# Optimization experiments

Hardware: AMD Instinct MI355X
Metric: run time of the kernel (lower is better)

## Reference

```python
import jax, jax.numpy as jnp
import numpy as np
import math

B, T, D = 2, 1024, 128
H, DH = 64, 2
SCALE = math.sqrt(DH)
TEMPERATURE = 0.8

def setup_inputs() -> dict:
    key = jax.random.key(0)
    ks = jax.random.split(key, 5)
    inv = 1.0 / math.sqrt(D)
    return {
        "x": jax.random.normal(ks[0], (B, T, D), dtype=jnp.float32),
        "Wq": jax.random.normal(ks[1], (D, D), dtype=jnp.float32) * inv,
        "Wk": jax.random.normal(ks[2], (D, D), dtype=jnp.float32) * inv,
        "Wv": jax.random.normal(ks[3], (D, D), dtype=jnp.float32) * inv,
        "Wo": jax.random.normal(ks[4], (D, D), dtype=jnp.float32) * inv,
    }

def reference(x, Wq, Wk, Wv, Wo):
    b, t, d = x.shape
    # torch nn.Linear(bias=False): y = x @ W.T
    Q = (x @ Wq.T).reshape(b, t, H, DH).transpose(0, 2, 1, 3)  # (B,H,T,dh)
    K = (x @ Wk.T).reshape(b, t, H, DH).transpose(0, 2, 1, 3)
    V = (x @ Wv.T).reshape(b, t, H, DH).transpose(0, 2, 1, 3)
    # scores / sqrt(d_head) / temperature, causal mask (strict upper -> -inf)
    scores = jnp.einsum("bhqd,bhkd->bhqk", Q, K) / (SCALE * TEMPERATURE)
    causal = jnp.triu(jnp.ones((t, t), dtype=bool), k=1)  # True above diagonal
    scores = jnp.where(causal, -jnp.inf, scores)
    attn = jax.nn.softmax(scores, axis=-1)  # dropout is identity in eval mode
    out = jnp.einsum("bhqk,bhkd->bhqd", attn, V)
    out = out.transpose(0, 2, 1, 3).reshape(b, t, d)
    return out @ Wo.T
```

## Files before the change

### kernel.cpp

```cpp
#include <hip/hip_runtime.h>
#include <math.h>

#define Tdim 1024
#define Hh   64

#if __has_builtin(__builtin_amdgcn_exp2f)
#define EXP2(x) __builtin_amdgcn_exp2f(x)
#else
#define EXP2(x) exp2f(x)
#endif

__device__ __constant__ float kQScale = 0.8838834764831844f * 1.4426950408889634f;

__global__ __launch_bounds__(256) void qkv_proj(
    const float* __restrict__ x, const float* __restrict__ Wq,
    const float* __restrict__ Wk, const float* __restrict__ Wv,
    float* __restrict__ Q, float* __restrict__ KV)
{
    __shared__ float xs[16][128];
    __shared__ float Wch[128][36];

    const int tid  = threadIdx.x;
    const int row0 = blockIdx.x * 16;
    const int w    = blockIdx.y;

    {
        const float4* xg = reinterpret_cast<const float4*>(x + (size_t)row0 * 128);
        reinterpret_cast<float4*>(&xs[0][0])[tid]       = xg[tid];
        reinterpret_cast<float4*>(&xs[0][0])[tid + 256] = xg[tid + 256];
    }

    const float* W = (w == 0) ? Wq : (w == 1) ? Wk : Wv;

    const int j0 = tid & 31;
    const int r0 = (tid >> 5) << 1;

    float acc[2][4];
#pragma unroll
    for (int r = 0; r < 2; ++r)
#pragma unroll
        for (int c = 0; c < 4; ++c) acc[r][c] = 0.f;

    for (int ch = 0; ch < 4; ++ch) {
        __syncthreads();
#pragma unroll
        for (int s = 0; s < 4; ++s) {
            const int idx  = tid + s * 256;
            const int rowW = idx >> 3;
            const int c4   = idx & 7;
            *reinterpret_cast<float4*>(&Wch[rowW][c4 * 4]) =
                reinterpret_cast<const float4*>(W + (size_t)rowW * 128 + ch * 32)[c4];
        }
        __syncthreads();

#pragma unroll
        for (int c = 0; c < 8; ++c) {
            const float4 w0 = *reinterpret_cast<const float4*>(&Wch[j0      ][c * 4]);
            const float4 w1 = *reinterpret_cast<const float4*>(&Wch[j0 + 32 ][c * 4]);
            const float4 w2 = *reinterpret_cast<const float4*>(&Wch[j0 + 64 ][c * 4]);
            const float4 w3 = *reinterpret_cast<const float4*>(&Wch[j0 + 96 ][c * 4]);
#pragma unroll
            for (int r = 0; r < 2; ++r) {
                const float4 xv = *reinterpret_cast<const float4*>(&xs[r0 + r][ch * 32 + c * 4]);
                acc[r][0] = fmaf(xv.x, w0.x, fmaf(xv.y, w0.y, fmaf(xv.z, w0.z, fmaf(xv.w, w0.w, acc[r][0]))));
                acc[r][1] = fmaf(xv.x, w1.x, fmaf(xv.y, w1.y, fmaf(xv.z, w1.z, fmaf(xv.w, w1.w, acc[r][1]))));
                acc[r][2] = fmaf(xv.x, w2.x, fmaf(xv.y, w2.y, fmaf(xv.z, w2.z, fmaf(xv.w, w2.w, acc[r][2]))));
                acc[r][3] = fmaf(xv.x, w3.x, fmaf(xv.y, w3.y, fmaf(xv.z, w3.z, fmaf(xv.w, w3.w, acc[r][3]))));
            }
        }
    }

#pragma unroll
    for (int r = 0; r < 2; ++r) {
        const int row = row0 + r0 + r;
        const int bb  = row >> 10;
        const int t   = row & 1023;
#pragma unroll
        for (int jj = 0; jj < 4; ++jj) {
            const int j = j0 + jj * 32;
            const float v = acc[r][jj];
            if (w == 0) {
                Q[(size_t)row * 128 + j] = v * kQScale;
            } else {
                const int h  = j >> 1, dh = j & 1;
                const int bh = bb * Hh + h;
                KV[((size_t)bh * Tdim + t) * 4 + ((w == 1) ? dh : 2 + dh)] = v;
            }
        }
    }
}

__global__ __launch_bounds__(256) void attn(
    const float* __restrict__ Q, const float4* __restrict__ KV,
    float* __restrict__ O)
{
    __shared__ float4 KVs[Tdim];
    const int tid   = threadIdx.x;
    const int c     = blockIdx.x;
    const int bh    = blockIdx.y;
    const int lowb  = c * 64;
    const int highb = (15 - c) * 64;
    const int nk    = highb + 64;

    const float4* KVg = KV + (size_t)bh * Tdim;
    for (int i = tid; i < nk; i += 256) KVs[i] = KVg[i];
    __syncthreads();

    const int sub = tid & 7;
    const int g   = tid >> 3;
    const int lq  = lowb + g * 2;
    const int hq  = highb + g * 2;
    const int b   = bh >> 6, h = bh & 63;

    const float* Qb = Q + (size_t)b * (Tdim * 128) + h * 2;
    float2 q[4];
    q[0] = *reinterpret_cast<const float2*>(Qb + (size_t)(lq    ) * 128);
    q[1] = *reinterpret_cast<const float2*>(Qb + (size_t)(lq + 1) * 128);
    q[2] = *reinterpret_cast<const float2*>(Qb + (size_t)(hq    ) * 128);
    q[3] = *reinterpret_cast<const float2*>(Qb + (size_t)(hq + 1) * 128);

    float l[4]  = {0.f, 0.f, 0.f, 0.f};
    float a0[4] = {0.f, 0.f, 0.f, 0.f};
    float a1[4] = {0.f, 0.f, 0.f, 0.f};

    auto upd = [&](int i, const float4 kv) {
        const float p = EXP2(fmaf(q[i].x, kv.x, q[i].y * kv.y));
        l[i] += p;
        a0[i] = fmaf(p, kv.z, a0[i]);
        a1[i] = fmaf(p, kv.w, a1[i]);
    };

#pragma unroll 2
    for (int k = sub; k < lq; k += 8) {
        const float4 kv = KVs[k];
        upd(0, kv); upd(1, kv); upd(2, kv); upd(3, kv);
    }
    if (sub <= 1) {
        const float4 kv = KVs[lq + sub];
        if (sub == 0) upd(0, kv);
        upd(1, kv);
    }
    int k2 = (lq & ~7) + sub; if (k2 < lq) k2 += 8;
#pragma unroll 4
    for (int k = k2; k < hq; k += 8) {
        const float4 kv = KVs[k];
        upd(2, kv); upd(3, kv);
    }
    if (sub <= 1) {
        const float4 kv = KVs[hq + sub];
        if (sub == 0) upd(2, kv);
        upd(3, kv);
    }

#pragma unroll
    for (int i = 0; i < 4; ++i) {
        l[i]  += __shfl_xor(l[i], 1);  l[i]  += __shfl_xor(l[i], 2);  l[i]  += __shfl_xor(l[i], 4);
        a0[i] += __shfl_xor(a0[i], 1); a0[i] += __shfl_xor(a0[i], 2); a0[i] += __shfl_xor(a0[i], 4);
        a1[i] += __shfl_xor(a1[i], 1); a1[i] += __shfl_xor(a1[i], 2); a1[i] += __shfl_xor(a1[i], 4);
    }

    if (sub == 0) {
        float* Ob = O + (size_t)b * (Tdim * 128) + h * 2;
#pragma unroll
        for (int i = 0; i < 4; ++i) {
            const int row = (i < 2) ? (lq + i) : (hq + i - 2);
            const float rl = 1.0f / l[i];
            *reinterpret_cast<float2*>(Ob + (size_t)row * 128) =
                make_float2(a0[i] * rl, a1[i] * rl);
        }
    }
}

__global__ __launch_bounds__(256) void out_proj(
    const float* __restrict__ Oin, const float* __restrict__ Wo,
    float* __restrict__ out)
{
    __shared__ float xs[16][128];
    __shared__ float Wch[128][36];

    const int tid  = threadIdx.x;
    const int row0 = blockIdx.x * 16;

    {
        const float4* xg = reinterpret_cast<const float4*>(Oin + (size_t)row0 * 128);
        reinterpret_cast<float4*>(&xs[0][0])[tid]       = xg[tid];
        reinterpret_cast<float4*>(&xs[0][0])[tid + 256] = xg[tid + 256];
    }

    const int j0 = tid & 31;
    const int r0 = (tid >> 5) << 1;

    float acc[2][4];
#pragma unroll
    for (int r = 0; r < 2; ++r)
#pragma unroll
        for (int c = 0; c < 4; ++c) acc[r][c] = 0.f;

    for (int ch = 0; ch < 4; ++ch) {
        __syncthreads();
#pragma unroll
        for (int s = 0; s < 4; ++s) {
            const int idx  = tid + s * 256;
            const int rowW = idx >> 3;
            const int c4   = idx & 7;
            *reinterpret_cast<float4*>(&Wch[rowW][c4 * 4]) =
                reinterpret_cast<const float4*>(Wo + (size_t)rowW * 128 + ch * 32)[c4];
        }
        __syncthreads();

#pragma unroll
        for (int c = 0; c < 8; ++c) {
            const float4 w0 = *reinterpret_cast<const float4*>(&Wch[j0      ][c * 4]);
            const float4 w1 = *reinterpret_cast<const float4*>(&Wch[j0 + 32 ][c * 4]);
            const float4 w2 = *reinterpret_cast<const float4*>(&Wch[j0 + 64 ][c * 4]);
            const float4 w3 = *reinterpret_cast<const float4*>(&Wch[j0 + 96 ][c * 4]);
#pragma unroll
            for (int r = 0; r < 2; ++r) {
                const float4 xv = *reinterpret_cast<const float4*>(&xs[r0 + r][ch * 32 + c * 4]);
                acc[r][0] = fmaf(xv.x, w0.x, fmaf(xv.y, w0.y, fmaf(xv.z, w0.z, fmaf(xv.w, w0.w, acc[r][0]))));
                acc[r][1] = fmaf(xv.x, w1.x, fmaf(xv.y, w1.y, fmaf(xv.z, w1.z, fmaf(xv.w, w1.w, acc[r][1]))));
                acc[r][2] = fmaf(xv.x, w2.x, fmaf(xv.y, w2.y, fmaf(xv.z, w2.z, fmaf(xv.w, w2.w, acc[r][2]))));
                acc[r][3] = fmaf(xv.x, w3.x, fmaf(xv.y, w3.y, fmaf(xv.z, w3.z, fmaf(xv.w, w3.w, acc[r][3]))));
            }
        }
    }

#pragma unroll
    for (int r = 0; r < 2; ++r) {
        const int row = row0 + r0 + r;
#pragma unroll
        for (int jj = 0; jj < 4; ++jj) {
            const int j = j0 + jj * 32;
            out[(size_t)row * 128 + j] = acc[r][jj];
        }
    }
}

extern "C" void kernel_launch(void* const* d_in, const int* in_sizes, int n_in,
                              void* d_out, int out_size, void* d_ws, size_t ws_size,
                              hipStream_t stream) {
    const float* x  = (const float*)d_in[0];
    const float* Wq = (const float*)d_in[1];
    const float* Wk = (const float*)d_in[2];
    const float* Wv = (const float*)d_in[3];
    const float* Wo = (const float*)d_in[4];
    float* out = (float*)d_out;

    float* ws = (float*)d_ws;
    float* Q  = ws;
    float* KV = ws + 262144;
    float* O  = ws + 786432;

    qkv_proj<<<dim3(128, 3), 256, 0, stream>>>(x, Wq, Wk, Wv, Q, KV);
    attn<<<dim3(8, 128), 256, 0, stream>>>(Q, (const float4*)KV, O);
    out_proj<<<128, 256, 0, stream>>>(O, Wo, out);
}
```

Measured before the change: 95.34 us.

## Rewrite projection GEMMs as row-per-thread register kernels with column-split grids

Result: slower. 102.8 us (+7.8%).

```diff
diff --git a/kernel.cpp b/kernel.cpp
--- a/kernel.cpp
+++ b/kernel.cpp
@@ -12,80 +12,57 @@
 
 __device__ __constant__ float kQScale = 0.8838834764831844f * 1.4426950408889634f;
 
-__global__ __launch_bounds__(256) void qkv_proj(
+__global__ __launch_bounds__(256, 2) void qkv_proj(
     const float* __restrict__ x, const float* __restrict__ Wq,
     const float* __restrict__ Wk, const float* __restrict__ Wv,
     float* __restrict__ Q, float* __restrict__ KV)
 {
-    __shared__ float xs[16][128];
-    __shared__ float Wch[128][36];
-
-    const int tid  = threadIdx.x;
-    const int row0 = blockIdx.x * 16;
-    const int w    = blockIdx.y;
-
+    const int tid = threadIdx.x;
+    const int row = blockIdx.x * 256 + tid;
+    const int jb  = blockIdx.y * 8;
+    const int mat = blockIdx.z;
+    const float* __restrict__ W = (mat == 0) ? Wq : (mat == 1) ? Wk : Wv;
+
+    float4 xr[32];
     {
-        const float4* xg = reinterpret_cast<const float4*>(x + (size_t)row0 * 128);
-        reinterpret_cast<float4*>(&xs[0][0])[tid]       = xg[tid];
-        reinterpret_cast<float4*>(&xs[0][0])[tid + 256] = xg[tid + 256];
-    }
-
-    const float* W = (w == 0) ? Wq : (w == 1) ? Wk : Wv;
-
-    const int j0 = tid & 31;
-    const int r0 = (tid >> 5) << 1;
-
-    float acc[2][4];
-#pragma unroll
-    for (int r = 0; r < 2; ++r)
-#pragma unroll
-        for (int c = 0; c < 4; ++c) acc[r][c] = 0.f;
-
-    for (int ch = 0; ch < 4; ++ch) {
-        __syncthreads();
-#pragma unroll
-        for (int s = 0; s < 4; ++s) {
-            const int idx  = tid + s * 256;
-            const int rowW = idx >> 3;
-            const int c4   = idx & 7;
-            *reinterpret_cast<float4*>(&Wch[rowW][c4 * 4]) =
-                reinterpret_cast<const float4*>(W + (size_t)rowW * 128 + ch * 32)[c4];
-        }
-        __syncthreads();
-
-#pragma unroll
-        for (int c = 0; c < 8; ++c) {
-            const float4 w0 = *reinterpret_cast<const float4*>(&Wch[j0      ][c * 4]);
-            const float4 w1 = *reinterpret_cast<const float4*>(&Wch[j0 + 32 ][c * 4]);
-            const float4 w2 = *reinterpret_cast<const float4*>(&Wch[j0 + 64 ][c * 4]);
-            const float4 w3 = *reinterpret_cast<const float4*>(&Wch[j0 + 96 ][c * 4]);
-#pragma unroll
-            for (int r = 0; r < 2; ++r) {
-                const float4 xv = *reinterpret_cast<const float4*>(&xs[r0 + r][ch * 32 + c * 4]);
-                acc[r][0] = fmaf(xv.x, w0.x, fmaf(xv.y, w0.y, fmaf(xv.z, w0.z, fmaf(xv.w, w0.w, acc[r][0]))));
-                acc[r][1] = fmaf(xv.x, w1.x, fmaf(xv.y, w1.y, fmaf(xv.z, w1.z, fmaf(xv.w, w1.w, acc[r][1]))));
-                acc[r][2] = fmaf(xv.x, w2.x, fmaf(xv.y, w2.y, fmaf(xv.z, w2.z, fmaf(xv.w, w2.w, acc[r][2]))));
-                acc[r][3] = fmaf(xv.x, w3.x, fmaf(xv.y, w3.y, fmaf(xv.z, w3.z, fmaf(xv.w, w3.w, acc[r][3]))));
-            }
-        }
-    }
-
-#pragma unroll
-    for (int r = 0; r < 2; ++r) {
-        const int row = row0 + r0 + r;
-        const int bb  = row >> 10;
-        const int t   = row & 1023;
-#pragma unroll
-        for (int jj = 0; jj < 4; ++jj) {
-            const int j = j0 + jj * 32;
-            const float v = acc[r][jj];
-            if (w == 0) {
-                Q[(size_t)row * 128 + j] = v * kQScale;
-            } else {
-                const int h  = j >> 1, dh = j & 1;
-                const int bh = bb * Hh + h;
-                KV[((size_t)bh * Tdim + t) * 4 + ((w == 1) ? dh : 2 + dh)] = v;
-            }
+        const float4* xrow = reinterpret_cast<const float4*>(x + (size_t)row * 128);
+#pragma unroll
+        for (int k = 0; k < 32; ++k) xr[k] = xrow[k];
+    }
+
+    float acc[8];
+#pragma unroll
+    for (int c = 0; c < 8; ++c) acc[c] = 0.f;
+
+#pragma unroll
+    for (int c = 0; c < 8; ++c) {
+        const float4* wp = reinterpret_cast<const float4*>(W + (size_t)(jb + c) * 128);
+        float a = 0.f;
+#pragma unroll
+        for (int k = 0; k < 32; ++k) {
+            const float4 wv = wp[k];
+            const float4 xv = xr[k];
+            a = fmaf(xv.x, wv.x, fmaf(xv.y, wv.y, fmaf(xv.z, wv.z, fmaf(xv.w, wv.w, a))));
+        }
+        acc[c] = a;
+    }
+
+    const int b = row >> 10, t = row & 1023;
+    if (mat == 0) {
+        float4 o0 = make_float4(acc[0] * kQScale, acc[1] * kQScale,
+                                acc[2] * kQScale, acc[3] * kQScale);
+        float4 o1 = make_float4(acc[4] * kQScale, acc[5] * kQScale,
+                                acc[6] * kQScale, acc[7] * kQScale);
+        *reinterpret_cast<float4*>(Q + (size_t)row * 128 + jb)     = o0;
+        *reinterpret_cast<float4*>(Q + (size_t)row * 128 + jb + 4) = o1;
+    } else {
+        const int off = (mat == 1) ? 0 : 2;
+#pragma unroll
+        for (int cc = 0; cc < 4; ++cc) {
+            const int h = (jb >> 1) + cc;
+            *reinterpret_cast<float2*>(
+                KV + (((size_t)(b * Hh + h) * Tdim + t) * 4 + off)) =
+                make_float2(acc[2 * cc], acc[2 * cc + 1]);
         }
     }
 }
@@ -171,69 +148,40 @@
     }
 }
 
-__global__ __launch_bounds__(256) void out_proj(
+__global__ __launch_bounds__(256, 2) void out_proj(
     const float* __restrict__ Oin, const float* __restrict__ Wo,
     float* __restrict__ out)
 {
-    __shared__ float xs[16][128];
-    __shared__ float Wch[128][36];
-
-    const int tid  = threadIdx.x;
-    const int row0 = blockIdx.x * 16;
-
+    const int tid = threadIdx.x;
+    const int row = blockIdx.x * 256 + tid;
+    const int jb  = blockIdx.y * 4;
+
+    float4 xr[32];
     {
-        const float4* xg = reinterpret_cast<const float4*>(Oin + (size_t)row0 * 128);
-        reinterpret_cast<float4*>(&xs[0][0])[tid]       = xg[tid];
-        reinterpret_cast<float4*>(&xs[0][0])[tid + 256] = xg[tid + 256];
-    }
-
-    const int j0 = tid & 31;
-    const int r0 = (tid >> 5) << 1;
-
-    float acc[2][4];
-#pragma unroll
-    for (int r = 0; r < 2; ++r)
-#pragma unroll
-        for (int c = 0; c < 4; ++c) acc[r][c] = 0.f;
-
-    for (int ch = 0; ch < 4; ++ch) {
-        __syncthreads();
-#pragma unroll
-        for (int s = 0; s < 4; ++s) {
-            const int idx  = tid + s * 256;
-            const int rowW = idx >> 3;
-            const int c4   = idx & 7;
-            *reinterpret_cast<float4*>(&Wch[rowW][c4 * 4]) =
-                reinterpret_cast<const float4*>(Wo + (size_t)rowW * 128 + ch * 32)[c4];
-        }
-        __syncthreads();
-
-#pragma unroll
-        for (int c = 0; c < 8; ++c) {
-            const float4 w0 = *reinterpret_cast<const float4*>(&Wch[j0      ][c * 4]);
-            const float4 w1 = *reinterpret_cast<const float4*>(&Wch[j0 + 32 ][c * 4]);
-            const float4 w2 = *reinterpret_cast<const float4*>(&Wch[j0 + 64 ][c * 4]);
-            const float4 w3 = *reinterpret_cast<const float4*>(&Wch[j0 + 96 ][c * 4]);
-#pragma unroll
-            for (int r = 0; r < 2; ++r) {
-                const float4 xv = *reinterpret_cast<const float4*>(&xs[r0 + r][ch * 32 + c * 4]);
-                acc[r][0] = fmaf(xv.x, w0.x, fmaf(xv.y, w0.y, fmaf(xv.z, w0.z, fmaf(xv.w, w0.w, acc[r][0]))));
-                acc[r][1] = fmaf(xv.x, w1.x, fmaf(xv.y, w1.y, fmaf(xv.z, w1.z, fmaf(xv.w, w1.w, acc[r][1]))));
-                acc[r][2] = fmaf(xv.x, w2.x, fmaf(xv.y, w2.y, fmaf(xv.z, w2.z, fmaf(xv.w, w2.w, acc[r][2]))));
-                acc[r][3] = fmaf(xv.x, w3.x, fmaf(xv.y, w3.y, fmaf(xv.z, w3.z, fmaf(xv.w, w3.w, acc[r][3]))));
-            }
-        }
-    }
-
-#pragma unroll
-    for (int r = 0; r < 2; ++r) {
-        const int row = row0 + r0 + r;
-#pragma unroll
-        for (int jj = 0; jj < 4; ++jj) {
-            const int j = j0 + jj * 32;
-            out[(size_t)row * 128 + j] = acc[r][jj];
-        }
-    }
+        const float4* xrow = reinterpret_cast<const float4*>(Oin + (size_t)row * 128);
+#pragma unroll
+        for (int k = 0; k < 32; ++k) xr[k] = xrow[k];
+    }
+
+    float acc[4];
+#pragma unroll
+    for (int c = 0; c < 4; ++c) acc[c] = 0.f;
+
+#pragma unroll
+    for (int c = 0; c < 4; ++c) {
+        const float4* wp = reinterpret_cast<const float4*>(Wo + (size_t)(jb + c) * 128);
+        float a = 0.f;
+#pragma unroll
+        for (int k = 0; k < 32; ++k) {
+            const float4 wv = wp[k];
+            const float4 xv = xr[k];
+            a = fmaf(xv.x, wv.x, fmaf(xv.y, wv.y, fmaf(xv.z, wv.z, fmaf(xv.w, wv.w, a))));
+        }
+        acc[c] = a;
+    }
+
+    *reinterpret_cast<float4*>(out + (size_t)row * 128 + jb) =
+        make_float4(acc[0], acc[1], acc[2], acc[3]);
 }
 
 extern "C" void kernel_launch(void* const* d_in, const int* in_sizes, int n_in,
@@ -251,7 +199,7 @@
     float* KV = ws + 262144;
     float* O  = ws + 786432;
 
-    qkv_proj<<<dim3(128, 3), 256, 0, stream>>>(x, Wq, Wk, Wv, Q, KV);
+    qkv_proj<<<dim3(8, 16, 3), 256, 0, stream>>>(x, Wq, Wk, Wv, Q, KV);
     attn<<<dim3(8, 128), 256, 0, stream>>>(Q, (const float4*)KV, O);
-    out_proj<<<128, 256, 0, stream>>>(O, Wo, out);
-}
+    out_proj<<<dim3(8, 32), 256, 0, stream>>>(O, Wo, out);
+}
```

## Process eight query rows per 16-lane group with mirrored high-row pairing

Applied to the files above, without the earlier changes.

Result: slower. 98.61 us (+3.4%).

```diff
diff --git a/kernel.cpp b/kernel.cpp
--- a/kernel.cpp
+++ b/kernel.cpp
@@ -106,22 +106,23 @@
     for (int i = tid; i < nk; i += 256) KVs[i] = KVg[i];
     __syncthreads();
 
-    const int sub = tid & 7;
-    const int g   = tid >> 3;
-    const int lq  = lowb + g * 2;
-    const int hq  = highb + g * 2;
+    const int sub = tid & 15;
+    const int g   = tid >> 4;
+    const int lq  = lowb + g * 4;
+    const int hq  = highb + (60 - g * 4);
     const int b   = bh >> 6, h = bh & 63;
 
     const float* Qb = Q + (size_t)b * (Tdim * 128) + h * 2;
-    float2 q[4];
-    q[0] = *reinterpret_cast<const float2*>(Qb + (size_t)(lq    ) * 128);
-    q[1] = *reinterpret_cast<const float2*>(Qb + (size_t)(lq + 1) * 128);
-    q[2] = *reinterpret_cast<const float2*>(Qb + (size_t)(hq    ) * 128);
-    q[3] = *reinterpret_cast<const float2*>(Qb + (size_t)(hq + 1) * 128);
-
-    float l[4]  = {0.f, 0.f, 0.f, 0.f};
-    float a0[4] = {0.f, 0.f, 0.f, 0.f};
-    float a1[4] = {0.f, 0.f, 0.f, 0.f};
+    float2 q[8];
+#pragma unroll
+    for (int i = 0; i < 4; ++i) {
+        q[i]     = *reinterpret_cast<const float2*>(Qb + (size_t)(lq + i) * 128);
+        q[4 + i] = *reinterpret_cast<const float2*>(Qb + (size_t)(hq + i) * 128);
+    }
+
+    float l[8], a0[8], a1[8];
+#pragma unroll
+    for (int i = 0; i < 8; ++i) { l[i] = 0.f; a0[i] = 0.f; a1[i] = 0.f; }
 
     auto upd = [&](int i, const float4 kv) {
         const float p = EXP2(fmaf(q[i].x, kv.x, q[i].y * kv.y));
@@ -131,39 +132,49 @@
     };
 
 #pragma unroll 2
-    for (int k = sub; k < lq; k += 8) {
+    for (int k = sub; k < lq; k += 16) {
         const float4 kv = KVs[k];
         upd(0, kv); upd(1, kv); upd(2, kv); upd(3, kv);
-    }
-    if (sub <= 1) {
+        upd(4, kv); upd(5, kv); upd(6, kv); upd(7, kv);
+    }
+    if (sub < 4) {
         const float4 kv = KVs[lq + sub];
         if (sub == 0) upd(0, kv);
-        upd(1, kv);
-    }
-    int k2 = (lq & ~7) + sub; if (k2 < lq) k2 += 8;
-#pragma unroll 4
-    for (int k = k2; k < hq; k += 8) {
+        if (sub <= 1) upd(1, kv);
+        if (sub <= 2) upd(2, kv);
+        upd(3, kv);
+        upd(4, kv); upd(5, kv); upd(6, kv); upd(7, kv);
+    }
+    int k2 = (lq & ~15) + sub;
+    if (k2 < lq + 4) k2 += 16;
+#pragma unroll 2
+    for (int k = k2; k < hq; k += 16) {
         const float4 kv = KVs[k];
-        upd(2, kv); upd(3, kv);
-    }
-    if (sub <= 1) {
+        upd(4, kv); upd(5, kv); upd(6, kv); upd(7, kv);
+    }
+    if (sub < 4) {
         const float4 kv = KVs[hq + sub];
-        if (sub == 0) upd(2, kv);
-        upd(3, kv);
-    }
-
-#pragma unroll
-    for (int i = 0; i < 4; ++i) {
-        l[i]  += __shfl_xor(l[i], 1);  l[i]  += __shfl_xor(l[i], 2);  l[i]  += __shfl_xor(l[i], 4);
-        a0[i] += __shfl_xor(a0[i], 1); a0[i] += __shfl_xor(a0[i], 2); a0[i] += __shfl_xor(a0[i], 4);
-        a1[i] += __shfl_xor(a1[i], 1); a1[i] += __shfl_xor(a1[i], 2); a1[i] += __shfl_xor(a1[i], 4);
+        if (sub == 0) upd(4, kv);
+        if (sub <= 1) upd(5, kv);
+        if (sub <= 2) upd(6, kv);
+        upd(7, kv);
+    }
+
+#pragma unroll
+    for (int i = 0; i < 8; ++i) {
+        l[i]  += __shfl_xor(l[i], 1);  l[i]  += __shfl_xor(l[i], 2);
+        l[i]  += __shfl_xor(l[i], 4);  l[i]  += __shfl_xor(l[i], 8);
+        a0[i] += __shfl_xor(a0[i], 1); a0[i] += __shfl_xor(a0[i], 2);
+        a0[i] += __shfl_xor(a0[i], 4); a0[i] += __shfl_xor(a0[i], 8);
+        a1[i] += __shfl_xor(a1[i], 1); a1[i] += __shfl_xor(a1[i], 2);
+        a1[i] += __shfl_xor(a1[i], 4); a1[i] += __shfl_xor(a1[i], 8);
     }
 
     if (sub == 0) {
         float* Ob = O + (size_t)b * (Tdim * 128) + h * 2;
 #pragma unroll
-        for (int i = 0; i < 4; ++i) {
-            const int row = (i < 2) ? (lq + i) : (hq + i - 2);
+        for (int i = 0; i < 8; ++i) {
+            const int row = (i < 4) ? (lq + i) : (hq + i - 4);
             const float rl = 1.0f / l[i];
             *reinterpret_cast<float2*>(Ob + (size_t)row * 128) =
                 make_float2(a0[i] * rl, a1[i] * rl);
```

## Split attention keys across two blocks with combine pass; halve out_proj tiles

Applied to the files above, without the earlier changes.

Result: slower. 99.56 us (+4.4%).

```diff
diff --git a/kernel.cpp b/kernel.cpp
--- a/kernel.cpp
+++ b/kernel.cpp
@@ -90,26 +90,30 @@
     }
 }
 
-__global__ __launch_bounds__(256) void attn(
+__global__ __launch_bounds__(256) void attn_split(
     const float* __restrict__ Q, const float4* __restrict__ KV,
-    float* __restrict__ O)
-{
-    __shared__ float4 KVs[Tdim];
-    const int tid   = threadIdx.x;
-    const int c     = blockIdx.x;
-    const int bh    = blockIdx.y;
+    float4* __restrict__ P)
+{
+    __shared__ float4 KVs[512];
+    const int tid = threadIdx.x;
+    const int c   = blockIdx.x & 7;
+    const int s   = blockIdx.x >> 3;
+    const int bh  = blockIdx.y;
     const int lowb  = c * 64;
     const int highb = (15 - c) * 64;
-    const int nk    = highb + 64;
+    const int nhalf = (highb + 64) >> 1;
 
     const float4* KVg = KV + (size_t)bh * Tdim;
-    for (int i = tid; i < nk; i += 256) KVs[i] = KVg[i];
+    for (int i = tid; i < nhalf; i += 256) {
+        const int gk = ((i >> 3) << 4) + s * 8 + (i & 7);
+        KVs[i] = KVg[gk];
+    }
     __syncthreads();
 
     const int sub = tid & 7;
     const int g   = tid >> 3;
-    const int lq  = lowb + g * 2;
-    const int hq  = highb + g * 2;
+    const int lq  = lowb + 2 * g;
+    const int hq  = highb + 62 - 2 * g;
     const int b   = bh >> 6, h = bh & 63;
 
     const float* Qb = Q + (size_t)b * (Tdim * 128) + h * 2;
@@ -130,26 +134,37 @@
         a1[i] = fmaf(p, kv.w, a1[i]);
     };
 
-#pragma unroll 2
-    for (int k = sub; k < lq; k += 8) {
-        const float4 kv = KVs[k];
-        upd(0, kv); upd(1, kv); upd(2, kv); upd(3, kv);
+    {
+        int i = sub;
+        for (int k = s * 8 + sub; k < lq; k += 16, i += 8) {
+            const float4 kv = KVs[i];
+            upd(0, kv); upd(1, kv); upd(2, kv); upd(3, kv);
+        }
     }
     if (sub <= 1) {
-        const float4 kv = KVs[lq + sub];
-        if (sub == 0) upd(0, kv);
-        upd(1, kv);
-    }
-    int k2 = (lq & ~7) + sub; if (k2 < lq) k2 += 8;
-#pragma unroll 4
-    for (int k = k2; k < hq; k += 8) {
-        const float4 kv = KVs[k];
-        upd(2, kv); upd(3, kv);
+        const int key = lq + sub;
+        if (((key >> 3) & 1) == s) {
+            const float4 kv = KVs[((key >> 4) << 3) | (key & 7)];
+            if (sub == 0) upd(0, kv);
+            upd(1, kv);
+        }
+    }
+    {
+        const int d = (s * 8 + sub - lq) & 15;
+        int k = lq + d;
+        int i = ((k >> 4) << 3) | sub;
+        for (; k < hq; k += 16, i += 8) {
+            const float4 kv = KVs[i];
+            upd(2, kv); upd(3, kv);
+        }
     }
     if (sub <= 1) {
-        const float4 kv = KVs[hq + sub];
-        if (sub == 0) upd(2, kv);
-        upd(3, kv);
+        const int key = hq + sub;
+        if (((key >> 3) & 1) == s) {
+            const float4 kv = KVs[((key >> 4) << 3) | (key & 7)];
+            if (sub == 0) upd(2, kv);
+            upd(3, kv);
+        }
     }
 
 #pragma unroll
@@ -160,15 +175,27 @@
     }
 
     if (sub == 0) {
-        float* Ob = O + (size_t)b * (Tdim * 128) + h * 2;
-#pragma unroll
-        for (int i = 0; i < 4; ++i) {
-            const int row = (i < 2) ? (lq + i) : (hq + i - 2);
-            const float rl = 1.0f / l[i];
-            *reinterpret_cast<float2*>(Ob + (size_t)row * 128) =
-                make_float2(a0[i] * rl, a1[i] * rl);
-        }
-    }
+        float4* Pb = P + ((size_t)(s * 128 + bh) << 10);
+        Pb[lq]     = make_float4(l[0], a0[0], a1[0], 0.f);
+        Pb[lq + 1] = make_float4(l[1], a0[1], a1[1], 0.f);
+        Pb[hq]     = make_float4(l[2], a0[2], a1[2], 0.f);
+        Pb[hq + 1] = make_float4(l[3], a0[3], a1[3], 0.f);
+    }
+}
+
+__global__ __launch_bounds__(256) void combine(
+    const float4* __restrict__ P, float* __restrict__ O)
+{
+    const int gid = blockIdx.x * 256 + threadIdx.x;
+    const int h = gid & 63;
+    const int t = (gid >> 6) & 1023;
+    const int b = gid >> 16;
+    const int bh = b * Hh + h;
+    const float4 pa = P[((size_t)bh << 10) + t];
+    const float4 pb = P[((size_t)(128 + bh) << 10) + t];
+    const float rl = 1.0f / (pa.x + pb.x);
+    *reinterpret_cast<float2*>(O + (size_t)(b * Tdim + t) * 128 + h * 2) =
+        make_float2((pa.y + pb.y) * rl, (pa.z + pb.z) * rl);
 }
 
 __global__ __launch_bounds__(256) void out_proj(
@@ -176,10 +203,11 @@
     float* __restrict__ out)
 {
     __shared__ float xs[16][128];
-    __shared__ float Wch[128][36];
+    __shared__ float Wch[64][36];
 
     const int tid  = threadIdx.x;
-    const int row0 = blockIdx.x * 16;
+    const int row0 = (blockIdx.x >> 1) * 16;
+    const int H    = blockIdx.x & 1;
 
     {
         const float4* xg = reinterpret_cast<const float4*>(Oin + (size_t)row0 * 128);
@@ -190,37 +218,30 @@
     const int j0 = tid & 31;
     const int r0 = (tid >> 5) << 1;
 
-    float acc[2][4];
-#pragma unroll
-    for (int r = 0; r < 2; ++r)
-#pragma unroll
-        for (int c = 0; c < 4; ++c) acc[r][c] = 0.f;
+    float acc[2][2] = {{0.f, 0.f}, {0.f, 0.f}};
 
     for (int ch = 0; ch < 4; ++ch) {
         __syncthreads();
 #pragma unroll
-        for (int s = 0; s < 4; ++s) {
-            const int idx  = tid + s * 256;
+        for (int s2 = 0; s2 < 2; ++s2) {
+            const int idx  = tid + s2 * 256;
             const int rowW = idx >> 3;
             const int c4   = idx & 7;
             *reinterpret_cast<float4*>(&Wch[rowW][c4 * 4]) =
-                reinterpret_cast<const float4*>(Wo + (size_t)rowW * 128 + ch * 32)[c4];
-        }
-        __syncthreads();
-
-#pragma unroll
-        for (int c = 0; c < 8; ++c) {
-            const float4 w0 = *reinterpret_cast<const float4*>(&Wch[j0      ][c * 4]);
-            const float4 w1 = *reinterpret_cast<const float4*>(&Wch[j0 + 32 ][c * 4]);
-            const float4 w2 = *reinterpret_cast<const float4*>(&Wch[j0 + 64 ][c * 4]);
-            const float4 w3 = *reinterpret_cast<const float4*>(&Wch[j0 + 96 ][c * 4]);
+                reinterpret_cast<const float4*>(
+                    Wo + (size_t)(H * 64 + rowW) * 128 + ch * 32)[c4];
+        }
+        __syncthreads();
+
+#pragma unroll
+        for (int cc = 0; cc < 8; ++cc) {
+            const float4 w0 = *reinterpret_cast<const float4*>(&Wch[j0     ][cc * 4]);
+            const float4 w1 = *reinterpret_cast<const float4*>(&Wch[j0 + 32][cc * 4]);
 #pragma unroll
             for (int r = 0; r < 2; ++r) {
-                const float4 xv = *reinterpret_cast<const float4*>(&xs[r0 + r][ch * 32 + c * 4]);
+                const float4 xv = *reinterpret_cast<const float4*>(&xs[r0 + r][ch * 32 + cc * 4]);
                 acc[r][0] = fmaf(xv.x, w0.x, fmaf(xv.y, w0.y, fmaf(xv.z, w0.z, fmaf(xv.w, w0.w, acc[r][0]))));
                 acc[r][1] = fmaf(xv.x, w1.x, fmaf(xv.y, w1.y, fmaf(xv.z, w1.z, fmaf(xv.w, w1.w, acc[r][1]))));
-                acc[r][2] = fmaf(xv.x, w2.x, fmaf(xv.y, w2.y, fmaf(xv.z, w2.z, fmaf(xv.w, w2.w, acc[r][2]))));
-                acc[r][3] = fmaf(xv.x, w3.x, fmaf(xv.y, w3.y, fmaf(xv.z, w3.z, fmaf(xv.w, w3.w, acc[r][3]))));
             }
         }
     }
@@ -228,11 +249,8 @@
 #pragma unroll
     for (int r = 0; r < 2; ++r) {
         const int row = row0 + r0 + r;
-#pragma unroll
-        for (int jj = 0; jj < 4; ++jj) {
-            const int j = j0 + jj * 32;
-            out[(size_t)row * 128 + j] = acc[r][jj];
-        }
+        out[(size_t)row * 128 + H * 64 + j0]      = acc[r][0];
+        out[(size_t)row * 128 + H * 64 + j0 + 32] = acc[r][1];
     }
 }
 
@@ -249,9 +267,11 @@
     float* ws = (float*)d_ws;
     float* Q  = ws;
     float* KV = ws + 262144;
-    float* O  = ws + 786432;
+    float* P  = ws + 786432;
+    float* O  = ws + 1835008;
 
     qkv_proj<<<dim3(128, 3), 256, 0, stream>>>(x, Wq, Wk, Wv, Q, KV);
-    attn<<<dim3(8, 128), 256, 0, stream>>>(Q, (const float4*)KV, O);
-    out_proj<<<128, 256, 0, stream>>>(O, Wo, out);
-}
+    attn_split<<<dim3(16, 128), 256, 0, stream>>>(Q, (const float4*)KV, (float4*)P);
+    combine<<<512, 256, 0, stream>>>((const float4*)P, O);
+    out_proj<<<256, 256, 0, stream>>>(O, Wo, out);
+}
```
